# Kernel optimization log

Hardware: AMD Instinct MI355X
Metric: run time of the kernel (lower is better)

## Reference

```python
import jax, jax.numpy as jnp
import numpy as np

WINDOW = 5
SIGMA = 4.0
KSIZE = 2 * int(4.0 * SIGMA + 0.5) + 1  # 33, matches torchvision GaussianBlur setup

H1, W1, B, N, C = 56, 56, 16, 32, 512
PAD = WINDOW - 1


def _gauss_kernel():
    x = jnp.arange(KSIZE, dtype=jnp.float32) - (KSIZE - 1) / 2.0
    k = jnp.exp(-0.5 * (x / SIGMA) ** 2)
    return k / jnp.sum(k)


def _blur(img):
    # separable Gaussian blur with reflect padding (torchvision GaussianBlur default)
    k = _gauss_kernel()
    p = KSIZE // 2
    x = jnp.pad(img, ((0, 0), (0, 0), (p, p), (p, p)), mode='reflect')
    dn = ('NCHW', 'OIHW', 'NCHW')
    x = jax.lax.conv_general_dilated(x, k.reshape(1, 1, KSIZE, 1), (1, 1), 'VALID', dimension_numbers=dn)
    x = jax.lax.conv_general_dilated(x, k.reshape(1, 1, 1, KSIZE), (1, 1), 'VALID', dimension_numbers=dn)
    return x


def _forward(embeddings, memory_bank, out_h, out_w):
    H, W, Bb, Cc = embeddings.shape
    x_norm = jnp.sum(embeddings * embeddings, axis=-1, keepdims=True)  # H W B 1
    best = None
    for d1 in range(WINDOW):
        for d2 in range(WINDOW):
            y = memory_bank[d1:H + d1, d2:W + d2]            # H W N C (shifted slice)
            y_norm = jnp.sum(y * y, axis=-1)                  # H W N
            cross = jnp.einsum('hwbc,hwnc->hwbn', embeddings, y)
            dsq = jnp.maximum(x_norm - 2.0 * cross + y_norm[:, :, None, :], 0.0)
            dmin = jnp.sqrt(jnp.min(dsq, axis=-1))            # H W B
            best = dmin if best is None else jnp.minimum(best, dmin)
    pix = jnp.transpose(best, (2, 0, 1))[:, None, :, :]        # B 1 H W
    img = jnp.max(pix, axis=(1, 2, 3))                         # B
    pix = jax.image.resize(pix, (Bb, 1, out_h, out_w), method='linear')  # align_corners=False bilinear
    return img, _blur(pix)


def setup_inputs() -> dict:
    key = jax.random.key(0)
    k1, k2 = jax.random.split(key)
    embeddings = jax.random.normal(k1, (H1, W1, B, C), dtype=jnp.float32)
    memory_bank = jax.random.normal(k2, (H1 + PAD, W1 + PAD, N, C), dtype=jnp.float32)
    return {'embeddings': embeddings, 'memory_bank': memory_bank, 'out_h': 224, 'out_w': 224}


def reference(embeddings, memory_bank, out_h, out_w):
    return _forward(embeddings, memory_bank, out_h, out_w)
```

## Files before the change

kernel.cpp:

```cpp
#include <hip/hip_runtime.h>
#include <math.h>

#define H1 56
#define W1 56
#define BB 16
#define NN 32
#define CC 512
#define MH 60
#define MW 60
#define OH 224
#define OW 224

typedef __bf16 bf16x8 __attribute__((ext_vector_type(8)));
typedef float floatx4 __attribute__((ext_vector_type(4)));

#define MBH_OFF   0
#define EMBH_OFF  29491200
#define F_XN_OFF  42336256
#define F_YN_OFF  42386432
#define F_BEST_OFF 42501632
#define F_TMP1_OFF 42551808
#define F_TOTAL_FLOATS 44157440ull

#define S_XN_OFF   0
#define S_YN_OFF   50176
#define S_BEST_OFF 165376
#define S_TMP1_OFF 215552

__global__ void cvt_norm_kernel(const float* __restrict__ src, __bf16* __restrict__ dsth,
                                float* __restrict__ norm, int nvec) {
    int wid  = (int)((blockIdx.x * blockDim.x + threadIdx.x) >> 6);
    int lane = threadIdx.x & 63;
    if (wid >= nvec) return;
    const float* p = src + (size_t)wid * CC + lane * 8;
    floatx4 a = *(const floatx4*)p;
    floatx4 b = *(const floatx4*)(p + 4);
    if (dsth) {
        bf16x8 v;
        v[0] = (__bf16)a.x; v[1] = (__bf16)a.y; v[2] = (__bf16)a.z; v[3] = (__bf16)a.w;
        v[4] = (__bf16)b.x; v[5] = (__bf16)b.y; v[6] = (__bf16)b.z; v[7] = (__bf16)b.w;
        *(bf16x8*)(dsth + (size_t)wid * CC + lane * 8) = v;
    }
    float s = a.x*a.x + a.y*a.y + a.z*a.z + a.w*a.w
            + b.x*b.x + b.y*b.y + b.z*b.z + b.w*b.w;
    s += __shfl_xor(s, 32, 64);
    s += __shfl_xor(s, 16, 64);
    s += __shfl_xor(s, 8, 64);
    s += __shfl_xor(s, 4, 64);
    s += __shfl_xor(s, 2, 64);
    s += __shfl_xor(s, 1, 64);
    if (lane == 0) norm[wid] = s;
}

#define BSTRIDE 520

__global__ __launch_bounds__(256, 2) void dist_kernel_bf16(
        const __bf16* __restrict__ embh, const __bf16* __restrict__ mbh,
        const float* __restrict__ xnorm, const float* __restrict__ ynorm,
        float* __restrict__ best) {
    __shared__ __bf16 Bs[NN * BSTRIDE];

    int bx   = blockIdx.x;
    int h0   = (bx / 14) * 2;
    int w0   = (bx % 14) * 4;
    int tid  = threadIdx.x;
    int wave = tid >> 6;
    int lane = tid & 63;
    int nrow = lane & 15;
    int seg  = lane >> 4;
    int w    = w0 + wave;

    bf16x8 afragA[16], afragB[16];
    const __bf16* apA = embh + ((size_t)(h0 * W1 + w) * BB + nrow) * CC + seg * 8;
    const __bf16* apB = embh + ((size_t)((h0 + 1) * W1 + w) * BB + nrow) * CC + seg * 8;
#pragma unroll
    for (int kk = 0; kk < 16; kk++) {
        afragA[kk] = *(const bf16x8*)(apA + kk * 32);
        afragB[kk] = *(const bf16x8*)(apB + kk * 32);
    }
    floatx4 xnA = *(const floatx4*)(xnorm + (size_t)(h0 * W1 + w) * BB + seg * 4);
    floatx4 xnB = *(const floatx4*)(xnorm + (size_t)((h0 + 1) * W1 + w) * BB + seg * 4);

    float bvA[4] = {1e30f, 1e30f, 1e30f, 1e30f};
    float bvB[4] = {1e30f, 1e30f, 1e30f, 1e30f};

    for (int rr = 0; rr < 6; rr++) {
        int mr = h0 + rr;
        for (int j = 0; j < 8; j++) {
            int mc = w0 + j;
            const __bf16* bp = mbh + (size_t)(mr * MW + mc) * NN * CC;
            __syncthreads();
#pragma unroll
            for (int t = 0; t < 8; t++) {
                int s  = t * 256 + tid;
                int n  = s >> 6;
                int ch = s & 63;
                *(bf16x8*)(&Bs[n * BSTRIDE + ch * 8]) = *(const bf16x8*)(bp + n * CC + ch * 8);
            }
            __syncthreads();

            int d2 = j - wave;
            if (d2 >= 0 && d2 < 5) {
                bool a0 = (rr < 5);
                bool a1 = (rr >= 1);
                float yn0 = ynorm[(size_t)(mr * MW + mc) * NN + nrow];
                float yn1 = ynorm[(size_t)(mr * MW + mc) * NN + nrow + 16];
                if (a0 && a1) {
                    floatx4 c0 = {0,0,0,0}, c1 = {0,0,0,0}, c2 = {0,0,0,0}, c3 = {0,0,0,0};
#pragma unroll
                    for (int kk = 0; kk < 16; kk++) {
                        bf16x8 b0 = *(const bf16x8*)(&Bs[nrow * BSTRIDE + kk * 32 + seg * 8]);
                        bf16x8 b1 = *(const bf16x8*)(&Bs[(nrow + 16) * BSTRIDE + kk * 32 + seg * 8]);
                        c0 = __builtin_amdgcn_mfma_f32_16x16x32_bf16(afragA[kk], b0, c0, 0, 0, 0);
                        c1 = __builtin_amdgcn_mfma_f32_16x16x32_bf16(afragA[kk], b1, c1, 0, 0, 0);
                        c2 = __builtin_amdgcn_mfma_f32_16x16x32_bf16(afragB[kk], b0, c2, 0, 0, 0);
                        c3 = __builtin_amdgcn_mfma_f32_16x16x32_bf16(afragB[kk], b1, c3, 0, 0, 0);
                    }
#pragma unroll
                    for (int r = 0; r < 4; r++) {
                        bvA[r] = fminf(bvA[r], fminf(fmaxf(xnA[r] - 2.f * c0[r] + yn0, 0.f),
                                                     fmaxf(xnA[r] - 2.f * c1[r] + yn1, 0.f)));
                        bvB[r] = fminf(bvB[r], fminf(fmaxf(xnB[r] - 2.f * c2[r] + yn0, 0.f),
                                                     fmaxf(xnB[r] - 2.f * c3[r] + yn1, 0.f)));
                    }
                } else if (a0) {
                    floatx4 c0 = {0,0,0,0}, c1 = {0,0,0,0};
#pragma unroll
                    for (int kk = 0; kk < 16; kk++) {
                        bf16x8 b0 = *(const bf16x8*)(&Bs[nrow * BSTRIDE + kk * 32 + seg * 8]);
                        bf16x8 b1 = *(const bf16x8*)(&Bs[(nrow + 16) * BSTRIDE + kk * 32 + seg * 8]);
                        c0 = __builtin_amdgcn_mfma_f32_16x16x32_bf16(afragA[kk], b0, c0, 0, 0, 0);
                        c1 = __builtin_amdgcn_mfma_f32_16x16x32_bf16(afragA[kk], b1, c1, 0, 0, 0);
                    }
#pragma unroll
                    for (int r = 0; r < 4; r++)
                        bvA[r] = fminf(bvA[r], fminf(fmaxf(xnA[r] - 2.f * c0[r] + yn0, 0.f),
                                                     fmaxf(xnA[r] - 2.f * c1[r] + yn1, 0.f)));
                } else {
                    floatx4 c2 = {0,0,0,0}, c3 = {0,0,0,0};
#pragma unroll
                    for (int kk = 0; kk < 16; kk++) {
                        bf16x8 b0 = *(const bf16x8*)(&Bs[nrow * BSTRIDE + kk * 32 + seg * 8]);
                        bf16x8 b1 = *(const bf16x8*)(&Bs[(nrow + 16) * BSTRIDE + kk * 32 + seg * 8]);
                        c2 = __builtin_amdgcn_mfma_f32_16x16x32_bf16(afragB[kk], b0, c2, 0, 0, 0);
                        c3 = __builtin_amdgcn_mfma_f32_16x16x32_bf16(afragB[kk], b1, c3, 0, 0, 0);
                    }
#pragma unroll
                    for (int r = 0; r < 4; r++)
                        bvB[r] = fminf(bvB[r], fminf(fmaxf(xnB[r] - 2.f * c2[r] + yn0, 0.f),
                                                     fmaxf(xnB[r] - 2.f * c3[r] + yn1, 0.f)));
                }
            }
        }
    }

#pragma unroll
    for (int r = 0; r < 4; r++) {
        float v = bvA[r];
        v = fminf(v, __shfl_xor(v, 1, 64));
        v = fminf(v, __shfl_xor(v, 2, 64));
        v = fminf(v, __shfl_xor(v, 4, 64));
        v = fminf(v, __shfl_xor(v, 8, 64));
        bvA[r] = v;
        float u = bvB[r];
        u = fminf(u, __shfl_xor(u, 1, 64));
        u = fminf(u, __shfl_xor(u, 2, 64));
        u = fminf(u, __shfl_xor(u, 4, 64));
        u = fminf(u, __shfl_xor(u, 8, 64));
        bvB[r] = u;
    }
    if ((lane & 15) == 0) {
        int posA = h0 * W1 + w;
        int posB = (h0 + 1) * W1 + w;
#pragma unroll
        for (int r = 0; r < 4; r++) {
            int b = seg * 4 + r;
            best[(size_t)b * (H1 * W1) + posA] = sqrtf(bvA[r]);
            best[(size_t)b * (H1 * W1) + posB] = sqrtf(bvB[r]);
        }
    }
}

__global__ __launch_bounds__(256) void dist_kernel_f32(
        const float* __restrict__ emb, const float* __restrict__ mb,
        const float* __restrict__ xnorm, const float* __restrict__ ynorm,
        float* __restrict__ best) {
    __shared__ __bf16 Bs[NN * BSTRIDE];
    int bx   = blockIdx.x;
    int h    = bx / 14;
    int w0   = (bx % 14) * 4;
    int tid  = threadIdx.x;
    int wave = tid >> 6;
    int lane = tid & 63;
    int nrow = lane & 15;
    int seg  = lane >> 4;
    int w    = w0 + wave;

    bf16x8 afrag[16];
    const float* ap = emb + ((size_t)(h * W1 + w) * BB + nrow) * CC + seg * 8;
#pragma unroll
    for (int kk = 0; kk < 16; kk++) {
        floatx4 f0 = *(const floatx4*)(ap + kk * 32);
        floatx4 f1 = *(const floatx4*)(ap + kk * 32 + 4);
        bf16x8 v;
        v[0] = (__bf16)f0.x; v[1] = (__bf16)f0.y; v[2] = (__bf16)f0.z; v[3] = (__bf16)f0.w;
        v[4] = (__bf16)f1.x; v[5] = (__bf16)f1.y; v[6] = (__bf16)f1.z; v[7] = (__bf16)f1.w;
        afrag[kk] = v;
    }
    floatx4 xn = *(const floatx4*)(xnorm + (size_t)(h * W1 + w) * BB + seg * 4);
    float bestv[4] = {1e30f, 1e30f, 1e30f, 1e30f};

    for (int d1 = 0; d1 < 5; d1++) {
        int mr = h + d1;
        for (int j = 0; j < 8; j++) {
            int mc = w0 + j;
            const float* bp = mb + (size_t)(mr * MW + mc) * NN * CC;
            __syncthreads();
#pragma unroll
            for (int t = 0; t < 8; t++) {
                int c0 = t * 256 + tid;
                int n  = c0 >> 6;
                int ks = (c0 & 63) << 3;
                floatx4 f0 = *(const floatx4*)(bp + n * CC + ks);
                floatx4 f1 = *(const floatx4*)(bp + n * CC + ks + 4);
                bf16x8 v;
                v[0] = (__bf16)f0.x; v[1] = (__bf16)f0.y; v[2] = (__bf16)f0.z; v[3] = (__bf16)f0.w;
                v[4] = (__bf16)f1.x; v[5] = (__bf16)f1.y; v[6] = (__bf16)f1.z; v[7] = (__bf16)f1.w;
                *(bf16x8*)(&Bs[n * BSTRIDE + ks]) = v;
            }
            __syncthreads();

            int d2 = j - wave;
            if (d2 >= 0 && d2 < 5) {
                float yn0 = ynorm[(size_t)(mr * MW + mc) * NN + nrow];
                float yn1 = ynorm[(size_t)(mr * MW + mc) * NN + nrow + 16];
                floatx4 acc0 = {0,0,0,0};
                floatx4 acc1 = {0,0,0,0};
#pragma unroll
                for (int kk = 0; kk < 16; kk++) {
                    bf16x8 b0 = *(const bf16x8*)(&Bs[nrow * BSTRIDE + kk * 32 + seg * 8]);
                    bf16x8 b1 = *(const bf16x8*)(&Bs[(nrow + 16) * BSTRIDE + kk * 32 + seg * 8]);
                    acc0 = __builtin_amdgcn_mfma_f32_16x16x32_bf16(afrag[kk], b0, acc0, 0, 0, 0);
                    acc1 = __builtin_amdgcn_mfma_f32_16x16x32_bf16(afrag[kk], b1, acc1, 0, 0, 0);
                }
#pragma unroll
                for (int r = 0; r < 4; r++) {
                    float d0  = fmaxf(xn[r] - 2.f * acc0[r] + yn0, 0.f);
                    float d1v = fmaxf(xn[r] - 2.f * acc1[r] + yn1, 0.f);
                    bestv[r] = fminf(bestv[r], fminf(d0, d1v));
                }
            }
        }
    }
#pragma unroll
    for (int r = 0; r < 4; r++) {
        float v = bestv[r];
        v = fminf(v, __shfl_xor(v, 1, 64));
        v = fminf(v, __shfl_xor(v, 2, 64));
        v = fminf(v, __shfl_xor(v, 4, 64));
        v = fminf(v, __shfl_xor(v, 8, 64));
        bestv[r] = v;
    }
    if ((lane & 15) == 0) {
        int pos = h * W1 + w;
#pragma unroll
        for (int r = 0; r < 4; r++) {
            int b = seg * 4 + r;
            best[(size_t)b * (H1 * W1) + pos] = sqrtf(bestv[r]);
        }
    }
}

__global__ void max_kernel(const float* __restrict__ best, float* __restrict__ out) {
    __shared__ float red[256];
    int b = blockIdx.x;
    float m = 0.f;
    for (int i = threadIdx.x; i < H1 * W1; i += 256)
        m = fmaxf(m, best[(size_t)b * (H1 * W1) + i]);
    red[threadIdx.x] = m;
    __syncthreads();
    for (int s = 128; s > 0; s >>= 1) {
        if (threadIdx.x < s) red[threadIdx.x] = fmaxf(red[threadIdx.x], red[threadIdx.x + s]);
        __syncthreads();
    }
    if (threadIdx.x == 0) out[b] = red[0];
}

struct GaussK { float k[33]; };

__device__ __forceinline__ int refl(int i, int n) {
    i = (i < 0) ? -i : i;
    i = (i > n - 1) ? 2 * (n - 1) - i : i;
    return i;
}

__global__ void vblur_kernel(const float* __restrict__ best, float* __restrict__ tmp1, GaussK g) {
    int idx = blockIdx.x * 256 + threadIdx.x;
    int lx = idx % W1;
    int y  = (idx / W1) % OH;
    int b  = idx / (W1 * OH);
    const float* p = best + (size_t)b * (H1 * W1);
    float acc = 0.f;
#pragma unroll
    for (int u = 0; u < 33; u++) {
        int z  = refl(y - 16 + u, OH);
        int rz = z & 3;
        float t = 0.125f + 0.25f * (float)((rz + 2) & 3);
        int lo = (z >> 2) + ((rz < 2) ? -1 : 0);
        int hi = min(lo + 1, H1 - 1);
        lo = max(lo, 0);
        acc += g.k[u] * ((1.f - t) * p[lo * W1 + lx] + t * p[hi * W1 + lx]);
    }
    tmp1[idx] = acc;
}

__global__ void hblur_kernel(const float* __restrict__ tmp1, float* __restrict__ dst, GaussK g) {
    int idx = blockIdx.x * 256 + threadIdx.x;
    int x = idx % OW;
    int y = (idx / OW) % OH;
    int b = idx / (OW * OH);
    const float* p = tmp1 + ((size_t)b * OH + y) * W1;
    float acc = 0.f;
#pragma unroll
    for (int u = 0; u < 33; u++) {
        int z  = refl(x - 16 + u, OW);
        int rz = z & 3;
        float t = 0.125f + 0.25f * (float)((rz + 2) & 3);
        int lo = (z >> 2) + ((rz < 2) ? -1 : 0);
        int hi = min(lo + 1, W1 - 1);
        lo = max(lo, 0);
        acc += g.k[u] * ((1.f - t) * p[lo] + t * p[hi]);
    }
    dst[idx] = acc;
}

extern "C" void kernel_launch(void* const* d_in, const int* in_sizes, int n_in,
                              void* d_out, int out_size, void* d_ws, size_t ws_size,
                              hipStream_t stream) {
    const float* emb = (const float*)d_in[0];
    const float* mbp = (const float*)d_in[1];
    float* ws  = (float*)d_ws;
    float* out = (float*)d_out;

    bool big = ws_size >= F_TOTAL_FLOATS * 4ull;

    float* xnorm = ws + (big ? F_XN_OFF   : S_XN_OFF);
    float* ynorm = ws + (big ? F_YN_OFF   : S_YN_OFF);
    float* best  = ws + (big ? F_BEST_OFF : S_BEST_OFF);
    float* tmp1  = ws + (big ? F_TMP1_OFF : S_TMP1_OFF);

    if (big) {
        __bf16* mbh  = (__bf16*)(ws + MBH_OFF);
        __bf16* embh = (__bf16*)(ws + EMBH_OFF);
        cvt_norm_kernel<<<(H1 * W1 * BB) / 4, 256, 0, stream>>>(emb, embh, xnorm, H1 * W1 * BB);
        cvt_norm_kernel<<<(MH * MW * NN) / 4, 256, 0, stream>>>(mbp, mbh, ynorm, MH * MW * NN);
        dist_kernel_bf16<<<28 * 14, 256, 0, stream>>>(embh, mbh, xnorm, ynorm, best);
    } else {
        cvt_norm_kernel<<<(H1 * W1 * BB) / 4, 256, 0, stream>>>(emb, nullptr, xnorm, H1 * W1 * BB);
        cvt_norm_kernel<<<(MH * MW * NN) / 4, 256, 0, stream>>>(mbp, nullptr, ynorm, MH * MW * NN);
        dist_kernel_f32<<<H1 * 14, 256, 0, stream>>>(emb, mbp, xnorm, ynorm, best);
    }

    max_kernel<<<BB, 256, 0, stream>>>(best, out);

    GaussK g;
    {
        double wsum = 0.0, wd[33];
        for (int u = 0; u < 33; u++) {
            double xk = (u - 16) / 4.0;
            wd[u] = exp(-0.5 * xk * xk);
            wsum += wd[u];
        }
        for (int u = 0; u < 33; u++) g.k[u] = (float)(wd[u] / wsum);
    }
    vblur_kernel<<<(BB * OH * W1) / 256, 256, 0, stream>>>(best, tmp1, g);
    hblur_kernel<<<(BB * OH * OW) / 256, 256, 0, stream>>>(tmp1, out + 16, g);
}
```

Measured before the change: 523.6 us.

## Double-buffer memory-bank tiles via direct global-to-LDS loads and fuse embedding conversion

The distance kernel now double-buffers memory-bank tiles in shared memory and uses global_load_lds to prefetch the next tile while MFMAs run on the current one. This halves the barriers per step and overlaps load latency with compute. The embedding bf16 conversion and norm computation move into the distance kernel, dropping one launch and an intermediate buffer. Block indices are also remapped to spread neighbouring tiles. The cost is doubled LDS use, which may limit occupancy. The direct-to-LDS copy also relies on its layout matching the padded BSTRIDE rows, with one 16-byte load per lane.

```diff
diff --git a/kernel.cpp b/kernel.cpp
--- a/kernel.cpp
+++ b/kernel.cpp
@@ -14,18 +14,20 @@
 typedef __bf16 bf16x8 __attribute__((ext_vector_type(8)));
 typedef float floatx4 __attribute__((ext_vector_type(4)));
 
-#define MBH_OFF   0
-#define EMBH_OFF  29491200
-#define F_XN_OFF  42336256
-#define F_YN_OFF  42386432
-#define F_BEST_OFF 42501632
-#define F_TMP1_OFF 42551808
-#define F_TOTAL_FLOATS 44157440ull
+#define MBH_OFF    0
+#define F_YN_OFF   29491200
+#define F_BEST_OFF 29606400
+#define F_TMP1_OFF 29656576
+#define F_TOTAL_FLOATS 29857280ull
 
 #define S_XN_OFF   0
 #define S_YN_OFF   50176
 #define S_BEST_OFF 165376
 #define S_TMP1_OFF 215552
+
+#define GLOAD_LDS16(g, l) __builtin_amdgcn_global_load_lds( \
+    (const __attribute__((address_space(1))) unsigned int*)(g), \
+    (__attribute__((address_space(3))) unsigned int*)(l), 16, 0, 0)
 
 __global__ void cvt_norm_kernel(const float* __restrict__ src, __bf16* __restrict__ dsth,
                                 float* __restrict__ norm, int nvec) {
@@ -55,12 +57,12 @@
 #define BSTRIDE 520
 
 __global__ __launch_bounds__(256, 2) void dist_kernel_bf16(
-        const __bf16* __restrict__ embh, const __bf16* __restrict__ mbh,
-        const float* __restrict__ xnorm, const float* __restrict__ ynorm,
-        float* __restrict__ best) {
-    __shared__ __bf16 Bs[NN * BSTRIDE];
-
-    int bx   = blockIdx.x;
+        const float* __restrict__ emb, const __bf16* __restrict__ mbh,
+        const float* __restrict__ ynorm, float* __restrict__ best) {
+    __shared__ __bf16 Bs[2][NN * BSTRIDE];
+
+    int bx0  = blockIdx.x;
+    int bx   = (bx0 & 7) * 49 + (bx0 >> 3);
     int h0   = (bx / 14) * 2;
     int w0   = (bx % 14) * 4;
     int tid  = threadIdx.x;
@@ -71,36 +73,68 @@
     int w    = w0 + wave;
 
     bf16x8 afragA[16], afragB[16];
-    const __bf16* apA = embh + ((size_t)(h0 * W1 + w) * BB + nrow) * CC + seg * 8;
-    const __bf16* apB = embh + ((size_t)((h0 + 1) * W1 + w) * BB + nrow) * CC + seg * 8;
+    float snA = 0.f, snB = 0.f;
+    const float* apA = emb + ((size_t)(h0 * W1 + w) * BB + nrow) * CC + seg * 8;
+    const float* apB = apA + (size_t)W1 * BB * CC;
 #pragma unroll
     for (int kk = 0; kk < 16; kk++) {
-        afragA[kk] = *(const bf16x8*)(apA + kk * 32);
-        afragB[kk] = *(const bf16x8*)(apB + kk * 32);
-    }
-    floatx4 xnA = *(const floatx4*)(xnorm + (size_t)(h0 * W1 + w) * BB + seg * 4);
-    floatx4 xnB = *(const floatx4*)(xnorm + (size_t)((h0 + 1) * W1 + w) * BB + seg * 4);
+        floatx4 a0 = *(const floatx4*)(apA + kk * 32);
+        floatx4 a1 = *(const floatx4*)(apA + kk * 32 + 4);
+        floatx4 b0 = *(const floatx4*)(apB + kk * 32);
+        floatx4 b1 = *(const floatx4*)(apB + kk * 32 + 4);
+        bf16x8 va, vb;
+        va[0] = (__bf16)a0.x; va[1] = (__bf16)a0.y; va[2] = (__bf16)a0.z; va[3] = (__bf16)a0.w;
+        va[4] = (__bf16)a1.x; va[5] = (__bf16)a1.y; va[6] = (__bf16)a1.z; va[7] = (__bf16)a1.w;
+        vb[0] = (__bf16)b0.x; vb[1] = (__bf16)b0.y; vb[2] = (__bf16)b0.z; vb[3] = (__bf16)b0.w;
+        vb[4] = (__bf16)b1.x; vb[5] = (__bf16)b1.y; vb[6] = (__bf16)b1.z; vb[7] = (__bf16)b1.w;
+        afragA[kk] = va; afragB[kk] = vb;
+        snA += a0.x*a0.x + a0.y*a0.y + a0.z*a0.z + a0.w*a0.w
+             + a1.x*a1.x + a1.y*a1.y + a1.z*a1.z + a1.w*a1.w;
+        snB += b0.x*b0.x + b0.y*b0.y + b0.z*b0.z + b0.w*b0.w
+             + b1.x*b1.x + b1.y*b1.y + b1.z*b1.z + b1.w*b1.w;
+    }
+    snA += __shfl_xor(snA, 16, 64); snA += __shfl_xor(snA, 32, 64);
+    snB += __shfl_xor(snB, 16, 64); snB += __shfl_xor(snB, 32, 64);
+    floatx4 xnA, xnB;
+#pragma unroll
+    for (int r = 0; r < 4; r++) {
+        xnA[r] = __shfl(snA, seg * 4 + r, 64);
+        xnB[r] = __shfl(snB, seg * 4 + r, 64);
+    }
 
     float bvA[4] = {1e30f, 1e30f, 1e30f, 1e30f};
     float bvB[4] = {1e30f, 1e30f, 1e30f, 1e30f};
 
+    {
+        const __bf16* bp = mbh + (size_t)(h0 * MW + w0) * NN * CC;
+#pragma unroll
+        for (int t = 0; t < 8; t++) {
+            int n = t * 4 + wave;
+            GLOAD_LDS16(bp + (size_t)n * CC + lane * 8, &Bs[0][n * BSTRIDE]);
+        }
+    }
+    __syncthreads();
+
+    int sidx = 0;
     for (int rr = 0; rr < 6; rr++) {
         int mr = h0 + rr;
-        for (int j = 0; j < 8; j++) {
+        for (int j = 0; j < 8; j++, sidx++) {
+            int cur = sidx & 1;
+            if (sidx + 1 < 48) {
+                int nrr = rr + ((j + 1) >> 3);
+                int nj  = (j + 1) & 7;
+                const __bf16* bp = mbh + (size_t)((h0 + nrr) * MW + (w0 + nj)) * NN * CC;
+#pragma unroll
+                for (int t = 0; t < 8; t++) {
+                    int n = t * 4 + wave;
+                    GLOAD_LDS16(bp + (size_t)n * CC + lane * 8, &Bs[cur ^ 1][n * BSTRIDE]);
+                }
+            }
+
             int mc = w0 + j;
-            const __bf16* bp = mbh + (size_t)(mr * MW + mc) * NN * CC;
-            __syncthreads();
-#pragma unroll
-            for (int t = 0; t < 8; t++) {
-                int s  = t * 256 + tid;
-                int n  = s >> 6;
-                int ch = s & 63;
-                *(bf16x8*)(&Bs[n * BSTRIDE + ch * 8]) = *(const bf16x8*)(bp + n * CC + ch * 8);
-            }
-            __syncthreads();
-
             int d2 = j - wave;
             if (d2 >= 0 && d2 < 5) {
+                const __bf16* Bc = &Bs[cur][0];
                 bool a0 = (rr < 5);
                 bool a1 = (rr >= 1);
                 float yn0 = ynorm[(size_t)(mr * MW + mc) * NN + nrow];
@@ -109,8 +143,8 @@
                     floatx4 c0 = {0,0,0,0}, c1 = {0,0,0,0}, c2 = {0,0,0,0}, c3 = {0,0,0,0};
 #pragma unroll
                     for (int kk = 0; kk < 16; kk++) {
-                        bf16x8 b0 = *(const bf16x8*)(&Bs[nrow * BSTRIDE + kk * 32 + seg * 8]);
-                        bf16x8 b1 = *(const bf16x8*)(&Bs[(nrow + 16) * BSTRIDE + kk * 32 + seg * 8]);
+                        bf16x8 b0 = *(const bf16x8*)(Bc + nrow * BSTRIDE + kk * 32 + seg * 8);
+                        bf16x8 b1 = *(const bf16x8*)(Bc + (nrow + 16) * BSTRIDE + kk * 32 + seg * 8);
                         c0 = __builtin_amdgcn_mfma_f32_16x16x32_bf16(afragA[kk], b0, c0, 0, 0, 0);
                         c1 = __builtin_amdgcn_mfma_f32_16x16x32_bf16(afragA[kk], b1, c1, 0, 0, 0);
                         c2 = __builtin_amdgcn_mfma_f32_16x16x32_bf16(afragB[kk], b0, c2, 0, 0, 0);
@@ -127,8 +161,8 @@
                     floatx4 c0 = {0,0,0,0}, c1 = {0,0,0,0};
 #pragma unroll
                     for (int kk = 0; kk < 16; kk++) {
-                        bf16x8 b0 = *(const bf16x8*)(&Bs[nrow * BSTRIDE + kk * 32 + seg * 8]);
-                        bf16x8 b1 = *(const bf16x8*)(&Bs[(nrow + 16) * BSTRIDE + kk * 32 + seg * 8]);
+                        bf16x8 b0 = *(const bf16x8*)(Bc + nrow * BSTRIDE + kk * 32 + seg * 8);
+                        bf16x8 b1 = *(const bf16x8*)(Bc + (nrow + 16) * BSTRIDE + kk * 32 + seg * 8);
                         c0 = __builtin_amdgcn_mfma_f32_16x16x32_bf16(afragA[kk], b0, c0, 0, 0, 0);
                         c1 = __builtin_amdgcn_mfma_f32_16x16x32_bf16(afragA[kk], b1, c1, 0, 0, 0);
                     }
@@ -140,8 +174,8 @@
                     floatx4 c2 = {0,0,0,0}, c3 = {0,0,0,0};
 #pragma unroll
                     for (int kk = 0; kk < 16; kk++) {
-                        bf16x8 b0 = *(const bf16x8*)(&Bs[nrow * BSTRIDE + kk * 32 + seg * 8]);
-                        bf16x8 b1 = *(const bf16x8*)(&Bs[(nrow + 16) * BSTRIDE + kk * 32 + seg * 8]);
+                        bf16x8 b0 = *(const bf16x8*)(Bc + nrow * BSTRIDE + kk * 32 + seg * 8);
+                        bf16x8 b1 = *(const bf16x8*)(Bc + (nrow + 16) * BSTRIDE + kk * 32 + seg * 8);
                         c2 = __builtin_amdgcn_mfma_f32_16x16x32_bf16(afragB[kk], b0, c2, 0, 0, 0);
                         c3 = __builtin_amdgcn_mfma_f32_16x16x32_bf16(afragB[kk], b1, c3, 0, 0, 0);
                     }
@@ -151,6 +185,7 @@
                                                      fmaxf(xnB[r] - 2.f * c3[r] + yn1, 0.f)));
                 }
             }
+            __syncthreads();
         }
     }
 
@@ -344,18 +379,21 @@
 
     bool big = ws_size >= F_TOTAL_FLOATS * 4ull;
 
-    float* xnorm = ws + (big ? F_XN_OFF   : S_XN_OFF);
-    float* ynorm = ws + (big ? F_YN_OFF   : S_YN_OFF);
-    float* best  = ws + (big ? F_BEST_OFF : S_BEST_OFF);
-    float* tmp1  = ws + (big ? F_TMP1_OFF : S_TMP1_OFF);
+    float* best;
+    float* tmp1;
 
     if (big) {
         __bf16* mbh  = (__bf16*)(ws + MBH_OFF);
-        __bf16* embh = (__bf16*)(ws + EMBH_OFF);
-        cvt_norm_kernel<<<(H1 * W1 * BB) / 4, 256, 0, stream>>>(emb, embh, xnorm, H1 * W1 * BB);
+        float* ynorm = ws + F_YN_OFF;
+        best = ws + F_BEST_OFF;
+        tmp1 = ws + F_TMP1_OFF;
         cvt_norm_kernel<<<(MH * MW * NN) / 4, 256, 0, stream>>>(mbp, mbh, ynorm, MH * MW * NN);
-        dist_kernel_bf16<<<28 * 14, 256, 0, stream>>>(embh, mbh, xnorm, ynorm, best);
+        dist_kernel_bf16<<<28 * 14, 256, 0, stream>>>(emb, mbh, ynorm, best);
     } else {
+        float* xnorm = ws + S_XN_OFF;
+        float* ynorm = ws + S_YN_OFF;
+        best = ws + S_BEST_OFF;
+        tmp1 = ws + S_TMP1_OFF;
         cvt_norm_kernel<<<(H1 * W1 * BB) / 4, 256, 0, stream>>>(emb, nullptr, xnorm, H1 * W1 * BB);
         cvt_norm_kernel<<<(MH * MW * NN) / 4, 256, 0, stream>>>(mbp, nullptr, ynorm, MH * MW * NN);
         dist_kernel_f32<<<H1 * 14, 256, 0, stream>>>(emb, mbp, xnorm, ynorm, best);
```

New measurement: 492.7 us, median of 2. 5.9% less time.
